# Performance work log

Measured on AMD Instinct MI355X. Metric: run time of the kernel, lower is better.

## Reference

```python
import jax, jax.numpy as jnp
import numpy as np

IN_DIM, HID, OUT_DIM, NUM_LAYERS = 768, 512, 768, 4
B, T = 128, 256
EPS = 1e-5


def setup_inputs() -> dict:
    key = jax.random.key(0)
    ks = jax.random.split(key, 16)
    s = 0.02
    inp = {
        "x": jax.random.normal(ks[0], (B, T, IN_DIM), dtype=jnp.float32),
        "h0": jnp.zeros((NUM_LAYERS, B, HID), dtype=jnp.float32),
        "c0": jnp.zeros((NUM_LAYERS, B, HID), dtype=jnp.float32),
        "W_in": jax.random.normal(ks[1], (HID, IN_DIM), dtype=jnp.float32) * s,
        "b_in": jnp.zeros((HID,), dtype=jnp.float32),
        # stacked LSTM weights: all layers take HID input (after input_proj)
        "W_ih": jax.random.normal(ks[2], (NUM_LAYERS, 4 * HID, HID), dtype=jnp.float32) * s,
        "W_hh": jax.random.normal(ks[3], (NUM_LAYERS, 4 * HID, HID), dtype=jnp.float32) * s,
        "b_ih": jnp.zeros((NUM_LAYERS, 4 * HID), dtype=jnp.float32),
        "b_hh": jnp.zeros((NUM_LAYERS, 4 * HID), dtype=jnp.float32),
        "W_out": jax.random.normal(ks[4], (OUT_DIM, HID), dtype=jnp.float32) * s,
        "b_out": jnp.zeros((OUT_DIM,), dtype=jnp.float32),
        "ln_g": jnp.ones((OUT_DIM,), dtype=jnp.float32),
        "ln_b": jnp.zeros((OUT_DIM,), dtype=jnp.float32),
    }
    return inp


def _lstm_layer(x_seq, h0, c0, Wih, Whh, bih, bhh):
    # x_seq: [B,T,H] -> outputs [B,T,H], (hT, cT)
    bias = bih + bhh  # fuse the two biases

    def step(carry, x_t):
        h, c = carry
        gates = x_t @ Wih.T + h @ Whh.T + bias  # [B,4H]
        i, f, g, o = jnp.split(gates, 4, axis=-1)  # PyTorch gate order i,f,g,o
        i = jax.nn.sigmoid(i)
        f = jax.nn.sigmoid(f)
        g = jnp.tanh(g)
        o = jax.nn.sigmoid(o)
        c = f * c + i * g
        h = o * jnp.tanh(c)
        return (h, c), h

    (hT, cT), hs = jax.lax.scan(step, (h0, c0), jnp.swapaxes(x_seq, 0, 1))
    return jnp.swapaxes(hs, 0, 1), hT, cT


def reference(x, h0, c0, W_in, b_in, W_ih, W_hh, b_ih, b_hh, W_out, b_out, ln_g, ln_b):
    # input projection
    h = x @ W_in.T + b_in  # [B,T,HID]
    h_finals, c_finals = [], []
    for l in range(NUM_LAYERS):  # fixed small layer count; dropout inactive (eval)
        h, hT, cT = _lstm_layer(h, h0[l], c0[l], W_ih[l], W_hh[l], b_ih[l], b_hh[l])
        h_finals.append(hT)
        c_finals.append(cT)
    out = h @ W_out.T + b_out  # [B,T,OUT]
    mu = jnp.mean(out, axis=-1, keepdims=True)
    var = jnp.mean(jnp.square(out - mu), axis=-1, keepdims=True)
    out = (out - mu) * jax.lax.rsqrt(var + EPS) * ln_g + ln_b
    return out, jnp.stack(h_finals), jnp.stack(c_finals)
```

## Files before the change

kernel.cpp:

```cpp
#include <hip/hip_runtime.h>
#include <math.h>

#define T_SEQ 256
#define BATCH 128
#define HID 512
#define NL 4
#define HT_OFF 25165824u
#define CT_OFF 25427968u
#define HALL_ELEMS 67371008u
#define XP_ELEMS   16777216u
#define FLG_OFF(l,t) ((((l) << 8) + (t)) << 6)

typedef __attribute__((ext_vector_type(8))) short bf16x8;
typedef __attribute__((ext_vector_type(4))) float f32x4;

#define GSTR 35

__device__ __forceinline__ short f2bf(float f) {
    unsigned u = __float_as_uint(f);
    u = (u + 0x7fffu + ((u >> 16) & 1u)) >> 16;
    return (short)u;
}
__device__ __forceinline__ unsigned pack2(float a, float b) {
    return ((unsigned)(unsigned short)f2bf(a)) |
           (((unsigned)(unsigned short)f2bf(b)) << 16);
}
__device__ __forceinline__ bf16x8 ld8_sc1g(const short* p) {
    unsigned long long q0 = __hip_atomic_load((const unsigned long long*)p,
                                              __ATOMIC_RELAXED, __HIP_MEMORY_SCOPE_AGENT);
    unsigned long long q1 = __hip_atomic_load((const unsigned long long*)(p + 512),
                                              __ATOMIC_RELAXED, __HIP_MEMORY_SCOPE_AGENT);
    union { unsigned long long q[2]; bf16x8 v; } u;
    u.q[0] = q0; u.q[1] = q1;
    return u.v;
}
__device__ __forceinline__ void poll_cnt4(const unsigned* base, int lane) {
    const unsigned* p = base + ((lane & 3) << 4);
    unsigned v = __hip_atomic_load(p, __ATOMIC_RELAXED, __HIP_MEMORY_SCOPE_AGENT);
    while (__any(v < 16u)) {
        __builtin_amdgcn_s_sleep(1);
        v = __hip_atomic_load(p, __ATOMIC_RELAXED, __HIP_MEMORY_SCOPE_AGENT);
    }
    asm volatile("" ::: "memory");
}
__device__ __forceinline__ void lds_wait(int* p, int want) {
    while (__hip_atomic_load(p, __ATOMIC_ACQUIRE, __HIP_MEMORY_SCOPE_WORKGROUP) < want)
        __builtin_amdgcn_s_sleep(1);
    asm volatile("" ::: "memory");
}
__device__ __forceinline__ float tanh_fast(float x) {
    float t = __expf(-2.f * fabsf(x));
    return copysignf((1.f - t) / (1.f + t), x);
}

__global__ void init_kernel(short* __restrict__ h_all, unsigned* __restrict__ flg,
                            const float* __restrict__ h0) {
    int idx = blockIdx.x * 256 + threadIdx.x;
    if (idx < NL * BATCH * HID) {
        int l = idx >> 16, rest = idx & 65535;
        int r = rest >> 9, k = rest & 511;
        h_all[((size_t)(l * 257) << 16) + (((size_t)(k >> 2)) << 9) + (r << 2) + (k & 3)]
            = f2bf(h0[idx]);
    }
    if (idx < NL * T_SEQ * 64) flg[idx] = 0u;
}

__global__ __launch_bounds__(256) void gemm_xp(const float* __restrict__ x,
                                               const float* __restrict__ W_in,
                                               const float* __restrict__ b_in,
                                               short* __restrict__ xp) {
    __shared__ short As[128 * 72];
    __shared__ short Bs[128 * 72];
    const int tid = threadIdx.x;
    const int w = tid >> 6, lane = tid & 63;
    const int m = lane & 15, quad = lane >> 4;
    const int rowbase = blockIdx.x * 128;
    const int colbase = blockIdx.y * 128;
    f32x4 acc[2][8];
#pragma unroll
    for (int rt = 0; rt < 2; ++rt)
#pragma unroll
        for (int ct = 0; ct < 8; ++ct) { f32x4 z = {0.f,0.f,0.f,0.f}; acc[rt][ct] = z; }

    for (int k0 = 0; k0 < 768; k0 += 64) {
        __syncthreads();
#pragma unroll
        for (int i = 0; i < 8; ++i) {
            int q = tid + (i << 8);
            int r = q >> 4, f4 = (q & 15) << 2;
            float4 v = *(const float4*)(x + (size_t)(rowbase + r) * 768 + k0 + f4);
            uint2 p; p.x = pack2(v.x, v.y); p.y = pack2(v.z, v.w);
            *(uint2*)&As[r * 72 + f4] = p;
        }
#pragma unroll
        for (int i = 0; i < 8; ++i) {
            int q = tid + (i << 8);
            int r = q >> 4, f4 = (q & 15) << 2;
            float4 v = *(const float4*)(W_in + (size_t)(colbase + r) * 768 + k0 + f4);
            uint2 p; p.x = pack2(v.x, v.y); p.y = pack2(v.z, v.w);
            *(uint2*)&Bs[r * 72 + f4] = p;
        }
        __syncthreads();
#pragma unroll
        for (int ks = 0; ks < 2; ++ks) {
            int kof = (ks << 5) + (quad << 3);
            bf16x8 a0 = *(const bf16x8*)&As[((w * 2 + 0) * 16 + m) * 72 + kof];
            bf16x8 a1 = *(const bf16x8*)&As[((w * 2 + 1) * 16 + m) * 72 + kof];
#pragma unroll
            for (int ct = 0; ct < 8; ++ct) {
                bf16x8 b = *(const bf16x8*)&Bs[(ct * 16 + m) * 72 + kof];
                acc[0][ct] = __builtin_amdgcn_mfma_f32_16x16x32_bf16(a0, b, acc[0][ct], 0, 0, 0);
                acc[1][ct] = __builtin_amdgcn_mfma_f32_16x16x32_bf16(a1, b, acc[1][ct], 0, 0, 0);
            }
        }
    }
    float bias_r[8];
#pragma unroll
    for (int ct = 0; ct < 8; ++ct) bias_r[ct] = b_in[colbase + ct * 16 + m];
#pragma unroll
    for (int rt = 0; rt < 2; ++rt)
#pragma unroll
        for (int reg = 0; reg < 4; ++reg) {
            int m_glob = rowbase + (w * 2 + rt) * 16 + quad * 4 + reg;
            int t = m_glob & 255, b = m_glob >> 8;
            short* dst = xp + (((size_t)(t << 7) + b) << 9);
#pragma unroll
            for (int ct = 0; ct < 8; ++ct)
                dst[colbase + ct * 16 + m] = f2bf(acc[rt][ct][reg] + bias_r[ct]);
        }
}

__global__ __launch_bounds__(256) void gemm_out(const short* __restrict__ h3,
                                                const float* __restrict__ W_out,
                                                const float* __restrict__ b_out,
                                                float* __restrict__ out) {
    __shared__ short As[128 * 72];
    __shared__ short Bs[128 * 72];
    const int tid = threadIdx.x;
    const int w = tid >> 6, lane = tid & 63;
    const int m = lane & 15, quad = lane >> 4;
    const int rowbase = blockIdx.x * 128;
    const int colbase = blockIdx.y * 128;
    f32x4 acc[2][8];
#pragma unroll
    for (int rt = 0; rt < 2; ++rt)
#pragma unroll
        for (int ct = 0; ct < 8; ++ct) { f32x4 z = {0.f,0.f,0.f,0.f}; acc[rt][ct] = z; }

    for (int k0 = 0; k0 < 512; k0 += 64) {
        __syncthreads();
#pragma unroll
        for (int i = 0; i < 4; ++i) {
            int q = tid + (i << 8);
            int r = q >> 3, seg = (q & 7) << 3;
            *(bf16x8*)&As[r * 72 + seg] =
                *(const bf16x8*)(h3 + (size_t)(rowbase + r) * 512 + k0 + seg);
        }
#pragma unroll
        for (int i = 0; i < 8; ++i) {
            int q = tid + (i << 8);
            int r = q >> 4, f4 = (q & 15) << 2;
            float4 v = *(const float4*)(W_out + (size_t)(colbase + r) * 512 + k0 + f4);
            uint2 p; p.x = pack2(v.x, v.y); p.y = pack2(v.z, v.w);
            *(uint2*)&Bs[r * 72 + f4] = p;
        }
        __syncthreads();
#pragma unroll
        for (int ks = 0; ks < 2; ++ks) {
            int kof = (ks << 5) + (quad << 3);
            bf16x8 a0 = *(const bf16x8*)&As[((w * 2 + 0) * 16 + m) * 72 + kof];
            bf16x8 a1 = *(const bf16x8*)&As[((w * 2 + 1) * 16 + m) * 72 + kof];
#pragma unroll
            for (int ct = 0; ct < 8; ++ct) {
                bf16x8 b = *(const bf16x8*)&Bs[(ct * 16 + m) * 72 + kof];
                acc[0][ct] = __builtin_amdgcn_mfma_f32_16x16x32_bf16(a0, b, acc[0][ct], 0, 0, 0);
                acc[1][ct] = __builtin_amdgcn_mfma_f32_16x16x32_bf16(a1, b, acc[1][ct], 0, 0, 0);
            }
        }
    }
    float bias_r[8];
#pragma unroll
    for (int ct = 0; ct < 8; ++ct) bias_r[ct] = b_out[colbase + ct * 16 + m];
#pragma unroll
    for (int rt = 0; rt < 2; ++rt)
#pragma unroll
        for (int reg = 0; reg < 4; ++reg) {
            int m_glob = rowbase + (w * 2 + rt) * 16 + quad * 4 + reg;
            int t = m_glob >> 7, b = m_glob & 127;
            float* dst = out + (size_t)b * 196608 + (size_t)t * 768;
#pragma unroll
            for (int ct = 0; ct < 8; ++ct)
                dst[colbase + ct * 16 + m] = acc[rt][ct][reg] + bias_r[ct];
        }
}

#define LOADQ(A0_, A1_, kb_)                                                  \
    _Pragma("unroll")                                                         \
    for (int kk = 0; kk < 4; ++kk) {                                          \
        int ks = (kb_) * 4 + kk;                                              \
        int g = ks * 8 + quad * 2;                                            \
        const short* pq = src + ((size_t)g << 9) + ((w2 * 32 + m) << 2);      \
        A0_[kk] = ld8_sc1g(pq);                                               \
        A1_[kk] = ld8_sc1g(pq + 64);                                          \
    }
#define COMPQ(A0_, A1_, kb_)                                                  \
    _Pragma("unroll")                                                         \
    for (int kk = 0; kk < 4; ++kk) {                                          \
        int ks = (kb_) * 4 + kk;                                              \
        acc00 = __builtin_amdgcn_mfma_f32_16x16x32_bf16(A0_[kk], wf[ks*2+0], acc00, 0, 0, 0); \
        acc01 = __builtin_amdgcn_mfma_f32_16x16x32_bf16(A0_[kk], wf[ks*2+1], acc01, 0, 0, 0); \
        acc10 = __builtin_amdgcn_mfma_f32_16x16x32_bf16(A1_[kk], wf[ks*2+0], acc10, 0, 0, 0); \
        acc11 = __builtin_amdgcn_mfma_f32_16x16x32_bf16(A1_[kk], wf[ks*2+1], acc11, 0, 0, 0); \
    }

__global__ __launch_bounds__(512, 1) void lstm_pipeline(
    short* __restrict__ xp, short* __restrict__ h_all,
    unsigned* __restrict__ flg,
    const float* __restrict__ W_ih, const float* __restrict__ W_hh,
    const float* __restrict__ b_ih, const float* __restrict__ b_hh,
    const float* __restrict__ c0, float* __restrict__ d_out) {
    __shared__ float gatesX[128 * GSTR];
    __shared__ float gatesH[128 * GSTR];
    __shared__ float cL[128 * 9];
    __shared__ float biasL[32];
    __shared__ int ldsdep[2];

    const int tid = threadIdx.x;
    const int l = blockIdx.x >> 6, c = blockIdx.x & 63;
    const int w = tid >> 6, lane = tid & 63;
    const int m = lane & 15, quad = lane >> 4;
    const bool hw = (w >= 4);
    const int w2 = w & 3;

    const float* Wsrc = hw ? W_hh : W_ih;
    bf16x8 wf[32];
#pragma unroll
    for (int ks = 0; ks < 16; ++ks) {
#pragma unroll
        for (int ct = 0; ct < 2; ++ct) {
            int u = ct * 16 + m;
            int gr = ((u >> 3) << 9) + (c << 3) + (u & 7);
            const float* s = Wsrc + ((size_t)(l * 2048 + gr) << 9) + ks * 32 + quad * 8;
            float4 v0 = *(const float4*)s;
            float4 v1 = *(const float4*)(s + 4);
            uint4 p;
            p.x = pack2(v0.x, v0.y); p.y = pack2(v0.z, v0.w);
            p.z = pack2(v1.x, v1.y); p.w = pack2(v1.z, v1.w);
            wf[ks * 2 + ct] = *(bf16x8*)&p;
        }
    }
    if (tid < 32) {
        int gr = ((tid >> 3) << 9) + (c << 3) + (tid & 7);
        biasL[tid] = b_ih[l * 2048 + gr] + b_hh[l * 2048 + gr];
    }
    if (tid < 2) ldsdep[tid] = 0;
    for (int p = tid; p < 1024; p += 512) {
        int r = p >> 3, hc = p & 7;
        cL[r * 9 + hc] = c0[((size_t)l << 16) + (r << 9) + (c << 3) + hc];
    }
    __syncthreads();

    const int er = tid >> 2, eq = (tid & 3) << 1;

    for (int t = 0; t < T_SEQ; ++t) {
        if (hw) {
            if (t > 0) {
                if (w == 4) {
                    poll_cnt4(flg + FLG_OFF(l, t - 1), lane);
                    __hip_atomic_store(&ldsdep[1], t, __ATOMIC_RELEASE,
                                       __HIP_MEMORY_SCOPE_WORKGROUP);
                } else {
                    lds_wait(&ldsdep[1], t);
                }
            }
        } else if (l > 0) {
            if (w == 0) {
                poll_cnt4(flg + FLG_OFF(l - 1, t), lane);
                __hip_atomic_store(&ldsdep[0], t + 1, __ATOMIC_RELEASE,
                                   __HIP_MEMORY_SCOPE_WORKGROUP);
            } else {
                lds_wait(&ldsdep[0], t + 1);
            }
        }
        asm volatile("" ::: "memory");

        f32x4 z = {0.f, 0.f, 0.f, 0.f};
        f32x4 acc00 = z, acc01 = z, acc10 = z, acc11 = z;

        if (!hw && l == 0) {
            const short* src = xp + ((size_t)t << 16);
#pragma unroll
            for (int ks = 0; ks < 16; ++ks) {
                int ka = ks * 32 + quad * 8;
                bf16x8 a0 = *(const bf16x8*)(src + ((size_t)(w2 * 32 + m) << 9) + ka);
                bf16x8 a1 = *(const bf16x8*)(src + ((size_t)(w2 * 32 + 16 + m) << 9) + ka);
                acc00 = __builtin_amdgcn_mfma_f32_16x16x32_bf16(a0, wf[ks * 2 + 0], acc00, 0, 0, 0);
                acc01 = __builtin_amdgcn_mfma_f32_16x16x32_bf16(a0, wf[ks * 2 + 1], acc01, 0, 0, 0);
                acc10 = __builtin_amdgcn_mfma_f32_16x16x32_bf16(a1, wf[ks * 2 + 0], acc10, 0, 0, 0);
                acc11 = __builtin_amdgcn_mfma_f32_16x16x32_bf16(a1, wf[ks * 2 + 1], acc11, 0, 0, 0);
            }
        } else {
            const short* src = hw
                ? (h_all + ((size_t)(l * 257 + t) << 16))
                : (h_all + ((size_t)((l - 1) * 257 + t + 1) << 16));
            bf16x8 Pa[4], Pb[4], Qa[4], Qb[4];
            LOADQ(Pa, Pb, 0)
            LOADQ(Qa, Qb, 1)
            COMPQ(Pa, Pb, 0)
            LOADQ(Pa, Pb, 2)
            COMPQ(Qa, Qb, 1)
            LOADQ(Qa, Qb, 3)
            COMPQ(Pa, Pb, 2)
            COMPQ(Qa, Qb, 3)
        }
        const int gb0 = w2 * 32 + quad * 4;
        float* gdst = hw ? gatesH : gatesX;
#pragma unroll
        for (int reg = 0; reg < 4; ++reg) {
            gdst[(gb0 + reg) * GSTR + m]           = acc00[reg];
            gdst[(gb0 + reg) * GSTR + 16 + m]      = acc01[reg];
            gdst[(gb0 + 16 + reg) * GSTR + m]      = acc10[reg];
            gdst[(gb0 + 16 + reg) * GSTR + 16 + m] = acc11[reg];
        }
        __syncthreads();

        float hv[2], cv[2];
#pragma unroll
        for (int e = 0; e < 2; ++e) {
            int hc = eq + e;
            float iv = gatesX[er * GSTR + hc]      + gatesH[er * GSTR + hc]      + biasL[hc];
            float fv = gatesX[er * GSTR + 8 + hc]  + gatesH[er * GSTR + 8 + hc]  + biasL[8 + hc];
            float gv = gatesX[er * GSTR + 16 + hc] + gatesH[er * GSTR + 16 + hc] + biasL[16 + hc];
            float ov = gatesX[er * GSTR + 24 + hc] + gatesH[er * GSTR + 24 + hc] + biasL[24 + hc];
            float ig = 1.f / (1.f + __expf(-iv));
            float fg = 1.f / (1.f + __expf(-fv));
            float gg = tanh_fast(gv);
            float og = 1.f / (1.f + __expf(-ov));
            float cn = fg * cL[er * 9 + hc] + ig * gg;
            float hn = og * tanh_fast(cn);
            cL[er * 9 + hc] = cn;
            hv[e] = hn; cv[e] = cn;
        }
        unsigned pk = pack2(hv[0], hv[1]);
        {
            int g = c * 2 + (eq >> 2);
            unsigned* hdst = (unsigned*)(h_all + ((size_t)(l * 257 + t + 1) << 16)
                                         + ((size_t)g << 9) + (er << 2) + (eq & 3));
            __hip_atomic_store(hdst, pk, __ATOMIC_RELAXED, __HIP_MEMORY_SCOPE_AGENT);
        }
        if (l == 3) {
            unsigned* xdst = (unsigned*)(xp + ((size_t)t << 16) + (er << 9) + (c << 3) + eq);
            __hip_atomic_store(xdst, pk, __ATOMIC_RELAXED, __HIP_MEMORY_SCOPE_AGENT);
        }
        if (t == T_SEQ - 1) {
            size_t fo = ((size_t)l << 16) + (size_t)(er << 9) + (c << 3) + eq;
            d_out[HT_OFF + fo]     = hv[0];
            d_out[HT_OFF + fo + 1] = hv[1];
            d_out[CT_OFF + fo]     = cv[0];
            d_out[CT_OFF + fo + 1] = cv[1];
        }
        __syncthreads();
        if (tid == 0)
            __hip_atomic_fetch_add(flg + FLG_OFF(l, t) + ((c >> 4) << 4), 1u,
                                   __ATOMIC_RELAXED, __HIP_MEMORY_SCOPE_AGENT);
    }
}

__global__ __launch_bounds__(256) void ln_kernel(float* __restrict__ out,
                                                 const float* __restrict__ g,
                                                 const float* __restrict__ bvec) {
    float* p = out + (size_t)blockIdx.x * 768;
    int tid = threadIdx.x;
    float v0 = p[tid], v1 = p[tid + 256], v2 = p[tid + 512];
    float s = v0 + v1 + v2;
    float q = v0 * v0 + v1 * v1 + v2 * v2;
    for (int off = 32; off > 0; off >>= 1) {
        s += __shfl_down(s, off);
        q += __shfl_down(q, off);
    }
    __shared__ float ss[4], qq[4];
    __shared__ float mu_s, rs_s;
    int w = tid >> 6;
    if ((tid & 63) == 0) { ss[w] = s; qq[w] = q; }
    __syncthreads();
    if (tid == 0) {
        float S = ss[0] + ss[1] + ss[2] + ss[3];
        float Q = qq[0] + qq[1] + qq[2] + qq[3];
        float mu = S * (1.f / 768.f);
        float var = Q * (1.f / 768.f) - mu * mu;
        mu_s = mu;
        rs_s = rsqrtf(var + 1e-5f);
    }
    __syncthreads();
    float mu = mu_s, rs = rs_s;
    p[tid]       = (v0 - mu) * rs * g[tid]       + bvec[tid];
    p[tid + 256] = (v1 - mu) * rs * g[tid + 256] + bvec[tid + 256];
    p[tid + 512] = (v2 - mu) * rs * g[tid + 512] + bvec[tid + 512];
}

extern "C" void kernel_launch(void* const* d_in, const int* in_sizes, int n_in,
                              void* d_out, int out_size, void* d_ws, size_t ws_size,
                              hipStream_t stream) {
    (void)in_sizes; (void)n_in; (void)out_size; (void)ws_size;
    const float* x     = (const float*)d_in[0];
    const float* h0    = (const float*)d_in[1];
    const float* c0    = (const float*)d_in[2];
    const float* W_in  = (const float*)d_in[3];
    const float* b_in  = (const float*)d_in[4];
    const float* W_ih  = (const float*)d_in[5];
    const float* W_hh  = (const float*)d_in[6];
    const float* b_ih  = (const float*)d_in[7];
    const float* b_hh  = (const float*)d_in[8];
    const float* W_out = (const float*)d_in[9];
    const float* b_out = (const float*)d_in[10];
    const float* ln_g  = (const float*)d_in[11];
    const float* ln_b  = (const float*)d_in[12];

    float* out   = (float*)d_out;
    short* h_all = (short*)d_ws;
    short* xp    = h_all + HALL_ELEMS;
    unsigned* flg = (unsigned*)(xp + XP_ELEMS);

    init_kernel<<<1024, 256, 0, stream>>>(h_all, flg, h0);
    gemm_xp<<<dim3(256, 4), 256, 0, stream>>>(x, W_in, b_in, xp);
    lstm_pipeline<<<256, 512, 0, stream>>>(xp, h_all, flg, W_ih, W_hh,
                                           b_ih, b_hh, c0, out);
    gemm_out<<<dim3(256, 6), 256, 0, stream>>>(xp, W_out, b_out, out);
    ln_kernel<<<32768, 256, 0, stream>>>(out, ln_g, ln_b);
}
```

Measured before the change: 2.894 ms.

## Decouple input-gate waves from recurrent waves with double-buffered LDS and counters

```diff
diff --git a/kernel.cpp b/kernel.cpp
--- a/kernel.cpp
+++ b/kernel.cpp
@@ -15,6 +15,7 @@
 typedef __attribute__((ext_vector_type(4))) float f32x4;
 
 #define GSTR 35
+#define WGSC __HIP_MEMORY_SCOPE_WORKGROUP
 
 __device__ __forceinline__ short f2bf(float f) {
     unsigned u = __float_as_uint(f);
@@ -37,14 +38,18 @@
 __device__ __forceinline__ void poll_cnt4(const unsigned* base, int lane) {
     const unsigned* p = base + ((lane & 3) << 4);
     unsigned v = __hip_atomic_load(p, __ATOMIC_RELAXED, __HIP_MEMORY_SCOPE_AGENT);
-    while (__any(v < 16u)) {
+    while (__any(v < 64u)) {
         __builtin_amdgcn_s_sleep(1);
         v = __hip_atomic_load(p, __ATOMIC_RELAXED, __HIP_MEMORY_SCOPE_AGENT);
     }
     asm volatile("" ::: "memory");
 }
-__device__ __forceinline__ void lds_wait(int* p, int want) {
-    while (__hip_atomic_load(p, __ATOMIC_ACQUIRE, __HIP_MEMORY_SCOPE_WORKGROUP) < want)
+__device__ __forceinline__ void spin_ge(int* p, int want) {
+    while (__hip_atomic_load(p, __ATOMIC_ACQUIRE, WGSC) < want) {}
+    asm volatile("" ::: "memory");
+}
+__device__ __forceinline__ void spin_ge_sleep(int* p, int want) {
+    while (__hip_atomic_load(p, __ATOMIC_ACQUIRE, WGSC) < want)
         __builtin_amdgcn_s_sleep(1);
     asm volatile("" ::: "memory");
 }
@@ -212,6 +217,14 @@
         acc10 = __builtin_amdgcn_mfma_f32_16x16x32_bf16(A1_[kk], wf[ks*2+0], acc10, 0, 0, 0); \
         acc11 = __builtin_amdgcn_mfma_f32_16x16x32_bf16(A1_[kk], wf[ks*2+1], acc11, 0, 0, 0); \
     }
+#define GWRITE(gdst_)                                                         \
+    _Pragma("unroll")                                                         \
+    for (int reg = 0; reg < 4; ++reg) {                                       \
+        (gdst_)[(gb0 + reg) * GSTR + m]           = acc00[reg];               \
+        (gdst_)[(gb0 + reg) * GSTR + 16 + m]      = acc01[reg];               \
+        (gdst_)[(gb0 + 16 + reg) * GSTR + m]      = acc10[reg];               \
+        (gdst_)[(gb0 + 16 + reg) * GSTR + 16 + m] = acc11[reg];               \
+    }
 
 __global__ __launch_bounds__(512, 1) void lstm_pipeline(
     short* __restrict__ xp, short* __restrict__ h_all,
@@ -219,11 +232,12 @@
     const float* __restrict__ W_ih, const float* __restrict__ W_hh,
     const float* __restrict__ b_ih, const float* __restrict__ b_hh,
     const float* __restrict__ c0, float* __restrict__ d_out) {
-    __shared__ float gatesX[128 * GSTR];
+    __shared__ float gatesX[2][128 * GSTR];
     __shared__ float gatesH[128 * GSTR];
     __shared__ float cL[128 * 9];
     __shared__ float biasL[32];
     __shared__ int ldsdep[2];
+    __shared__ int xb, hb1, hb2;
 
     const int tid = threadIdx.x;
     const int l = blockIdx.x >> 6, c = blockIdx.x & 63;
@@ -254,115 +268,139 @@
         biasL[tid] = b_ih[l * 2048 + gr] + b_hh[l * 2048 + gr];
     }
     if (tid < 2) ldsdep[tid] = 0;
+    if (tid == 2) { xb = 0; }
+    if (tid == 3) { hb1 = 0; }
+    if (tid == 4) { hb2 = 0; }
     for (int p = tid; p < 1024; p += 512) {
         int r = p >> 3, hc = p & 7;
         cL[r * 9 + hc] = c0[((size_t)l << 16) + (r << 9) + (c << 3) + hc];
     }
     __syncthreads();
 
-    const int er = tid >> 2, eq = (tid & 3) << 1;
-
-    for (int t = 0; t < T_SEQ; ++t) {
-        if (hw) {
+    if (!hw) {
+        for (int t = 0; t < T_SEQ; ++t) {
+            if (l > 0) {
+                if (w == 0) {
+                    poll_cnt4(flg + FLG_OFF(l - 1, t), lane);
+                    __hip_atomic_store(&ldsdep[0], t + 1, __ATOMIC_RELEASE, WGSC);
+                } else {
+                    spin_ge_sleep(&ldsdep[0], t + 1);
+                }
+            }
+            f32x4 z = {0.f, 0.f, 0.f, 0.f};
+            f32x4 acc00 = z, acc01 = z, acc10 = z, acc11 = z;
+            if (l == 0) {
+                const short* src = xp + ((size_t)t << 16);
+#pragma unroll
+                for (int ks = 0; ks < 16; ++ks) {
+                    int ka = ks * 32 + quad * 8;
+                    bf16x8 a0 = *(const bf16x8*)(src + ((size_t)(w2 * 32 + m) << 9) + ka);
+                    bf16x8 a1 = *(const bf16x8*)(src + ((size_t)(w2 * 32 + 16 + m) << 9) + ka);
+                    acc00 = __builtin_amdgcn_mfma_f32_16x16x32_bf16(a0, wf[ks * 2 + 0], acc00, 0, 0, 0);
+                    acc01 = __builtin_amdgcn_mfma_f32_16x16x32_bf16(a0, wf[ks * 2 + 1], acc01, 0, 0, 0);
+                    acc10 = __builtin_amdgcn_mfma_f32_16x16x32_bf16(a1, wf[ks * 2 + 0], acc10, 0, 0, 0);
+                    acc11 = __builtin_amdgcn_mfma_f32_16x16x32_bf16(a1, wf[ks * 2 + 1], acc11, 0, 0, 0);
+                }
+            } else {
+                const short* src = h_all + ((size_t)((l - 1) * 257 + t + 1) << 16);
+                bf16x8 Pa[4], Pb[4], Qa[4], Qb[4];
+                LOADQ(Pa, Pb, 0)
+                LOADQ(Qa, Qb, 1)
+                COMPQ(Pa, Pb, 0)
+                LOADQ(Pa, Pb, 2)
+                COMPQ(Qa, Qb, 1)
+                LOADQ(Qa, Qb, 3)
+                COMPQ(Pa, Pb, 2)
+                COMPQ(Qa, Qb, 3)
+            }
+            if (t >= 2) spin_ge_sleep(&hb2, 4 * (t - 1));
+            float* gX = gatesX[t & 1];
+            const int gb0 = w2 * 32 + quad * 4;
+            GWRITE(gX)
+            if (lane == 0)
+                __hip_atomic_fetch_add(&xb, 1, __ATOMIC_ACQ_REL, WGSC);
+        }
+    } else {
+        __builtin_amdgcn_s_setprio(1);
+        const int ht = tid - 256, er = ht >> 1, eq0 = (ht & 1) * 4;
+        for (int t = 0; t < T_SEQ; ++t) {
             if (t > 0) {
                 if (w == 4) {
                     poll_cnt4(flg + FLG_OFF(l, t - 1), lane);
-                    __hip_atomic_store(&ldsdep[1], t, __ATOMIC_RELEASE,
-                                       __HIP_MEMORY_SCOPE_WORKGROUP);
+                    __hip_atomic_store(&ldsdep[1], t, __ATOMIC_RELEASE, WGSC);
                 } else {
-                    lds_wait(&ldsdep[1], t);
+                    spin_ge_sleep(&ldsdep[1], t);
                 }
             }
-        } else if (l > 0) {
-            if (w == 0) {
-                poll_cnt4(flg + FLG_OFF(l - 1, t), lane);
-                __hip_atomic_store(&ldsdep[0], t + 1, __ATOMIC_RELEASE,
-                                   __HIP_MEMORY_SCOPE_WORKGROUP);
-            } else {
-                lds_wait(&ldsdep[0], t + 1);
-            }
-        }
-        asm volatile("" ::: "memory");
-
-        f32x4 z = {0.f, 0.f, 0.f, 0.f};
-        f32x4 acc00 = z, acc01 = z, acc10 = z, acc11 = z;
-
-        if (!hw && l == 0) {
-            const short* src = xp + ((size_t)t << 16);
-#pragma unroll
-            for (int ks = 0; ks < 16; ++ks) {
-                int ka = ks * 32 + quad * 8;
-                bf16x8 a0 = *(const bf16x8*)(src + ((size_t)(w2 * 32 + m) << 9) + ka);
-                bf16x8 a1 = *(const bf16x8*)(src + ((size_t)(w2 * 32 + 16 + m) << 9) + ka);
-                acc00 = __builtin_amdgcn_mfma_f32_16x16x32_bf16(a0, wf[ks * 2 + 0], acc00, 0, 0, 0);
-                acc01 = __builtin_amdgcn_mfma_f32_16x16x32_bf16(a0, wf[ks * 2 + 1], acc01, 0, 0, 0);
-                acc10 = __builtin_amdgcn_mfma_f32_16x16x32_bf16(a1, wf[ks * 2 + 0], acc10, 0, 0, 0);
-                acc11 = __builtin_amdgcn_mfma_f32_16x16x32_bf16(a1, wf[ks * 2 + 1], acc11, 0, 0, 0);
-            }
-        } else {
-            const short* src = hw
-                ? (h_all + ((size_t)(l * 257 + t) << 16))
-                : (h_all + ((size_t)((l - 1) * 257 + t + 1) << 16));
-            bf16x8 Pa[4], Pb[4], Qa[4], Qb[4];
-            LOADQ(Pa, Pb, 0)
-            LOADQ(Qa, Qb, 1)
-            COMPQ(Pa, Pb, 0)
-            LOADQ(Pa, Pb, 2)
-            COMPQ(Qa, Qb, 1)
-            LOADQ(Qa, Qb, 3)
-            COMPQ(Pa, Pb, 2)
-            COMPQ(Qa, Qb, 3)
-        }
-        const int gb0 = w2 * 32 + quad * 4;
-        float* gdst = hw ? gatesH : gatesX;
-#pragma unroll
-        for (int reg = 0; reg < 4; ++reg) {
-            gdst[(gb0 + reg) * GSTR + m]           = acc00[reg];
-            gdst[(gb0 + reg) * GSTR + 16 + m]      = acc01[reg];
-            gdst[(gb0 + 16 + reg) * GSTR + m]      = acc10[reg];
-            gdst[(gb0 + 16 + reg) * GSTR + 16 + m] = acc11[reg];
-        }
-        __syncthreads();
-
-        float hv[2], cv[2];
-#pragma unroll
-        for (int e = 0; e < 2; ++e) {
-            int hc = eq + e;
-            float iv = gatesX[er * GSTR + hc]      + gatesH[er * GSTR + hc]      + biasL[hc];
-            float fv = gatesX[er * GSTR + 8 + hc]  + gatesH[er * GSTR + 8 + hc]  + biasL[8 + hc];
-            float gv = gatesX[er * GSTR + 16 + hc] + gatesH[er * GSTR + 16 + hc] + biasL[16 + hc];
-            float ov = gatesX[er * GSTR + 24 + hc] + gatesH[er * GSTR + 24 + hc] + biasL[24 + hc];
-            float ig = 1.f / (1.f + __expf(-iv));
-            float fg = 1.f / (1.f + __expf(-fv));
-            float gg = tanh_fast(gv);
-            float og = 1.f / (1.f + __expf(-ov));
-            float cn = fg * cL[er * 9 + hc] + ig * gg;
-            float hn = og * tanh_fast(cn);
-            cL[er * 9 + hc] = cn;
-            hv[e] = hn; cv[e] = cn;
-        }
-        unsigned pk = pack2(hv[0], hv[1]);
-        {
-            int g = c * 2 + (eq >> 2);
-            unsigned* hdst = (unsigned*)(h_all + ((size_t)(l * 257 + t + 1) << 16)
-                                         + ((size_t)g << 9) + (er << 2) + (eq & 3));
-            __hip_atomic_store(hdst, pk, __ATOMIC_RELAXED, __HIP_MEMORY_SCOPE_AGENT);
-        }
-        if (l == 3) {
-            unsigned* xdst = (unsigned*)(xp + ((size_t)t << 16) + (er << 9) + (c << 3) + eq);
-            __hip_atomic_store(xdst, pk, __ATOMIC_RELAXED, __HIP_MEMORY_SCOPE_AGENT);
-        }
-        if (t == T_SEQ - 1) {
-            size_t fo = ((size_t)l << 16) + (size_t)(er << 9) + (c << 3) + eq;
-            d_out[HT_OFF + fo]     = hv[0];
-            d_out[HT_OFF + fo + 1] = hv[1];
-            d_out[CT_OFF + fo]     = cv[0];
-            d_out[CT_OFF + fo + 1] = cv[1];
-        }
-        __syncthreads();
-        if (tid == 0)
-            __hip_atomic_fetch_add(flg + FLG_OFF(l, t) + ((c >> 4) << 4), 1u,
-                                   __ATOMIC_RELAXED, __HIP_MEMORY_SCOPE_AGENT);
+            f32x4 z = {0.f, 0.f, 0.f, 0.f};
+            f32x4 acc00 = z, acc01 = z, acc10 = z, acc11 = z;
+            {
+                const short* src = h_all + ((size_t)(l * 257 + t) << 16);
+                bf16x8 Pa[4], Pb[4], Qa[4], Qb[4];
+                LOADQ(Pa, Pb, 0)
+                LOADQ(Qa, Qb, 1)
+                COMPQ(Pa, Pb, 0)
+                LOADQ(Pa, Pb, 2)
+                COMPQ(Qa, Qb, 1)
+                LOADQ(Qa, Qb, 3)
+                COMPQ(Pa, Pb, 2)
+                COMPQ(Qa, Qb, 3)
+            }
+            const int gb0 = w2 * 32 + quad * 4;
+            GWRITE(gatesH)
+            if (lane == 0)
+                __hip_atomic_fetch_add(&hb1, 1, __ATOMIC_ACQ_REL, WGSC);
+            spin_ge(&hb1, 4 * (t + 1));
+            spin_ge(&xb, 4 * (t + 1));
+            const float* gX = gatesX[t & 1];
+
+            float hv[4], cv[4];
+#pragma unroll
+            for (int e = 0; e < 4; ++e) {
+                int hc = eq0 + e;
+                float iv = gX[er * GSTR + hc]      + gatesH[er * GSTR + hc]      + biasL[hc];
+                float fv = gX[er * GSTR + 8 + hc]  + gatesH[er * GSTR + 8 + hc]  + biasL[8 + hc];
+                float gv = gX[er * GSTR + 16 + hc] + gatesH[er * GSTR + 16 + hc] + biasL[16 + hc];
+                float ov = gX[er * GSTR + 24 + hc] + gatesH[er * GSTR + 24 + hc] + biasL[24 + hc];
+                float ig = 1.f / (1.f + __expf(-iv));
+                float fg = 1.f / (1.f + __expf(-fv));
+                float gg = tanh_fast(gv);
+                float og = 1.f / (1.f + __expf(-ov));
+                float cn = fg * cL[er * 9 + hc] + ig * gg;
+                float hn = og * tanh_fast(cn);
+                cL[er * 9 + hc] = cn;
+                hv[e] = hn; cv[e] = cn;
+            }
+            unsigned long long pk;
+            {
+                union { unsigned u[2]; unsigned long long q; } uu;
+                uu.u[0] = pack2(hv[0], hv[1]); uu.u[1] = pack2(hv[2], hv[3]);
+                pk = uu.q;
+            }
+            {
+                int g = c * 2 + (ht & 1);
+                unsigned long long* hdst =
+                    (unsigned long long*)(h_all + ((size_t)(l * 257 + t + 1) << 16)
+                                          + ((size_t)g << 9) + (er << 2));
+                __hip_atomic_store(hdst, pk, __ATOMIC_RELAXED, __HIP_MEMORY_SCOPE_AGENT);
+            }
+            if (l == 3) {
+                unsigned long long* xdst =
+                    (unsigned long long*)(xp + ((size_t)t << 16) + (er << 9) + (c << 3) + eq0);
+                __hip_atomic_store(xdst, pk, __ATOMIC_RELAXED, __HIP_MEMORY_SCOPE_AGENT);
+            }
+            if (t == T_SEQ - 1) {
+                size_t fo = ((size_t)l << 16) + (size_t)(er << 9) + (c << 3) + eq0;
+                *(float4*)(d_out + HT_OFF + fo) = make_float4(hv[0], hv[1], hv[2], hv[3]);
+                *(float4*)(d_out + CT_OFF + fo) = make_float4(cv[0], cv[1], cv[2], cv[3]);
+            }
+            asm volatile("s_waitcnt vmcnt(0)" ::: "memory");
+            if (lane == 0) {
+                __hip_atomic_fetch_add(flg + FLG_OFF(l, t) + ((c >> 4) << 4), 1u,
+                                       __ATOMIC_RELAXED, __HIP_MEMORY_SCOPE_AGENT);
+                __hip_atomic_fetch_add(&hb2, 1, __ATOMIC_RELEASE, WGSC);
+            }
+        }
     }
 }
 
```

Result: slower. 4.838 ms (+67.1%).

## Replace counter flags with per-block flags and plain loads behind an acquire fence

Applied to the files above, without the earlier changes.

```diff
diff --git a/kernel.cpp b/kernel.cpp
--- a/kernel.cpp
+++ b/kernel.cpp
@@ -15,6 +15,7 @@
 typedef __attribute__((ext_vector_type(4))) float f32x4;
 
 #define GSTR 35
+#define WGSC __HIP_MEMORY_SCOPE_WORKGROUP
 
 __device__ __forceinline__ short f2bf(float f) {
     unsigned u = __float_as_uint(f);
@@ -25,26 +26,27 @@
     return ((unsigned)(unsigned short)f2bf(a)) |
            (((unsigned)(unsigned short)f2bf(b)) << 16);
 }
-__device__ __forceinline__ bf16x8 ld8_sc1g(const short* p) {
-    unsigned long long q0 = __hip_atomic_load((const unsigned long long*)p,
-                                              __ATOMIC_RELAXED, __HIP_MEMORY_SCOPE_AGENT);
-    unsigned long long q1 = __hip_atomic_load((const unsigned long long*)(p + 512),
-                                              __ATOMIC_RELAXED, __HIP_MEMORY_SCOPE_AGENT);
+__device__ __forceinline__ bf16x8 ld8_pln(const short* p) {
     union { unsigned long long q[2]; bf16x8 v; } u;
-    u.q[0] = q0; u.q[1] = q1;
+    u.q[0] = *(const unsigned long long*)p;
+    u.q[1] = *(const unsigned long long*)(p + 512);
     return u.v;
 }
-__device__ __forceinline__ void poll_cnt4(const unsigned* base, int lane) {
-    const unsigned* p = base + ((lane & 3) << 4);
+__device__ __forceinline__ void acq_fence() {
+    __builtin_amdgcn_fence(__ATOMIC_ACQUIRE, "agent");
+    asm volatile("" ::: "memory");
+}
+__device__ __forceinline__ void poll_flags64(const unsigned* base, int lane) {
+    const unsigned* p = base + lane;
     unsigned v = __hip_atomic_load(p, __ATOMIC_RELAXED, __HIP_MEMORY_SCOPE_AGENT);
-    while (__any(v < 16u)) {
+    while (__any(v == 0u)) {
         __builtin_amdgcn_s_sleep(1);
         v = __hip_atomic_load(p, __ATOMIC_RELAXED, __HIP_MEMORY_SCOPE_AGENT);
     }
     asm volatile("" ::: "memory");
 }
 __device__ __forceinline__ void lds_wait(int* p, int want) {
-    while (__hip_atomic_load(p, __ATOMIC_ACQUIRE, __HIP_MEMORY_SCOPE_WORKGROUP) < want)
+    while (__hip_atomic_load(p, __ATOMIC_ACQUIRE, WGSC) < want)
         __builtin_amdgcn_s_sleep(1);
     asm volatile("" ::: "memory");
 }
@@ -200,8 +202,8 @@
         int ks = (kb_) * 4 + kk;                                              \
         int g = ks * 8 + quad * 2;                                            \
         const short* pq = src + ((size_t)g << 9) + ((w2 * 32 + m) << 2);      \
-        A0_[kk] = ld8_sc1g(pq);                                               \
-        A1_[kk] = ld8_sc1g(pq + 64);                                          \
+        A0_[kk] = ld8_pln(pq);                                                \
+        A1_[kk] = ld8_pln(pq + 64);                                           \
     }
 #define COMPQ(A0_, A1_, kb_)                                                  \
     _Pragma("unroll")                                                         \
@@ -266,23 +268,21 @@
         if (hw) {
             if (t > 0) {
                 if (w == 4) {
-                    poll_cnt4(flg + FLG_OFF(l, t - 1), lane);
-                    __hip_atomic_store(&ldsdep[1], t, __ATOMIC_RELEASE,
-                                       __HIP_MEMORY_SCOPE_WORKGROUP);
+                    poll_flags64(flg + FLG_OFF(l, t - 1), lane);
+                    __hip_atomic_store(&ldsdep[1], t, __ATOMIC_RELEASE, WGSC);
                 } else {
                     lds_wait(&ldsdep[1], t);
                 }
             }
         } else if (l > 0) {
             if (w == 0) {
-                poll_cnt4(flg + FLG_OFF(l - 1, t), lane);
-                __hip_atomic_store(&ldsdep[0], t + 1, __ATOMIC_RELEASE,
-                                   __HIP_MEMORY_SCOPE_WORKGROUP);
+                poll_flags64(flg + FLG_OFF(l - 1, t), lane);
+                __hip_atomic_store(&ldsdep[0], t + 1, __ATOMIC_RELEASE, WGSC);
             } else {
                 lds_wait(&ldsdep[0], t + 1);
             }
         }
-        asm volatile("" ::: "memory");
+        acq_fence();
 
         f32x4 z = {0.f, 0.f, 0.f, 0.f};
         f32x4 acc00 = z, acc01 = z, acc10 = z, acc11 = z;
@@ -348,6 +348,10 @@
                                          + ((size_t)g << 9) + (er << 2) + (eq & 3));
             __hip_atomic_store(hdst, pk, __ATOMIC_RELAXED, __HIP_MEMORY_SCOPE_AGENT);
         }
+        __syncthreads();
+        if (tid == 0)
+            __hip_atomic_store(flg + FLG_OFF(l, t) + c, 1u,
+                               __ATOMIC_RELAXED, __HIP_MEMORY_SCOPE_AGENT);
         if (l == 3) {
             unsigned* xdst = (unsigned*)(xp + ((size_t)t << 16) + (er << 9) + (c << 3) + eq);
             __hip_atomic_store(xdst, pk, __ATOMIC_RELAXED, __HIP_MEMORY_SCOPE_AGENT);
@@ -359,10 +363,6 @@
             d_out[CT_OFF + fo]     = cv[0];
             d_out[CT_OFF + fo + 1] = cv[1];
         }
-        __syncthreads();
-        if (tid == 0)
-            __hip_atomic_fetch_add(flg + FLG_OFF(l, t) + ((c >> 4) << 4), 1u,
-                                   __ATOMIC_RELAXED, __HIP_MEMORY_SCOPE_AGENT);
     }
 }
 
```

After: 5.688 ms. 1.97x slower.
